# Optimization experiments

Measured on AMD Instinct MI355X. Metric: run time of the kernel, lower is better.

## Reference

```python
import jax, jax.numpy as jnp
import numpy as np

B, N, N_IN, MSG_HID, MSG_OUT, N_HID, N_OUT, K = 32, 128, 16, 64, 64, 64, 16, 4
E = N * (N - 1)  # 16256 directed edges, fully connected w/o self-loops


def setup_inputs() -> dict:
    key = jax.random.key(0)
    ks = jax.random.split(key, 8)
    # one-hot relation matrices (NRI convention)
    rows, cols = np.where(np.ones((N, N)) - np.eye(N))
    eye = np.eye(N, dtype=np.float32)
    rel_rec = jnp.asarray(eye[rows])   # [E, N]
    rel_send = jnp.asarray(eye[cols])  # [E, N]
    s = 0.1  # weight init scale
    return {
        "inputs": jax.random.normal(ks[0], (B, N_IN, N), jnp.float32),
        "rel_rec": rel_rec,
        "rel_send": rel_send,
        "rel_types": jax.nn.softmax(jax.random.normal(ks[1], (B, E, K), jnp.float32), axis=-1),
        "W1": jax.random.normal(ks[2], (K, 2 * N_IN, MSG_HID), jnp.float32) * s,
        "b1": jnp.zeros((K, MSG_HID), jnp.float32),
        "W2": jax.random.normal(ks[3], (K, MSG_HID, MSG_OUT), jnp.float32) * s,
        "b2": jnp.zeros((K, MSG_OUT), jnp.float32),
        "Wo1": jax.random.normal(ks[4], (MSG_OUT + N_IN, N_HID), jnp.float32) * s,
        "bo1": jnp.zeros((N_HID,), jnp.float32),
        "Wo2": jax.random.normal(ks[5], (N_HID, N_HID), jnp.float32) * s,
        "bo2": jnp.zeros((N_HID,), jnp.float32),
        "Wo3": jax.random.normal(ks[6], (N_HID, N_OUT), jnp.float32) * s,
        "bo3": jnp.zeros((N_OUT,), jnp.float32),
    }


def reference(inputs, rel_rec, rel_send, rel_types, W1, b1, W2, b2, Wo1, bo1, Wo2, bo2, Wo3, bo3):
    x = jnp.transpose(inputs, (0, 2, 1))                     # [B, N, n_in]
    senders = jnp.einsum('en,bnf->bef', rel_send, x)          # [B, E, n_in]
    receivers = jnp.einsum('en,bnf->bef', rel_rec, x)         # [B, E, n_in]
    pre_msg = jnp.concatenate([senders, receivers], axis=-1)  # [B, E, 2*n_in]
    all_msgs = jnp.zeros((pre_msg.shape[0], pre_msg.shape[1], W2.shape[-1]), pre_msg.dtype)
    for k in range(W1.shape[0]):  # small fixed loop over edge types
        m = jax.nn.relu(pre_msg @ W1[k] + b1[k])
        m = jax.nn.relu(m @ W2[k] + b2[k])
        all_msgs = all_msgs + m * rel_types[:, :, k:k + 1]
    # edge2node aggregation (no normalization in forward path, matches source)
    agg_msgs = jnp.einsum('bem,en->bnm', all_msgs, rel_rec)   # [B, N, msg_out]
    aug_msgs = jnp.concatenate([x, agg_msgs], axis=-1)        # [B, N, n_in+msg_out]
    h = jax.nn.relu(aug_msgs @ Wo1 + bo1)  # dropout disabled (eval mode)
    h = jax.nn.relu(h @ Wo2 + bo2)
    pred = h @ Wo3 + bo3                                      # [B, N, n_out]
    return jnp.transpose(pred, (0, 2, 1))                     # [B, n_out, N]
```

## Files before the change

### kernel.cpp

```cpp
#include <hip/hip_runtime.h>
#include <stdint.h>

#define B_  32
#define N_  128
#define NIN 16
#define K_  4
#define E_  (N_*(N_-1))

typedef float    f4 __attribute__((ext_vector_type(4)));
typedef _Float16 h8 __attribute__((ext_vector_type(8)));

__global__ __launch_bounds__(256) void prep(
    const float* __restrict__ inp, const float* __restrict__ W1,
    const float* __restrict__ b1,  const float* __restrict__ W2,
    const float* __restrict__ rt,
    _Float16* __restrict__ Sh, _Float16* __restrict__ Rh,
    _Float16* __restrict__ w2h, float* __restrict__ rtp)
{
    const int bid = blockIdx.x;
    const int tid = threadIdx.x;
    if (bid < 4096) {
        int gid = bid*256 + tid;
        int c = gid & 63;
        int n = (gid >> 6) & 127;
        int b = (gid >> 13) & 31;
        int k = gid >> 18;
        float s = 0.f, r = 0.f;
        const float* w1s = W1 + (k*32)*64 + c;
        const float* w1r = W1 + (k*32 + 16)*64 + c;
        const float* xp  = inp + (b*NIN)*N_ + n;
        #pragma unroll
        for (int f = 0; f < 16; ++f) {
            float xv = xp[f*N_];
            s += xv * w1s[f*64];
            r += xv * w1r[f*64];
        }
        r += b1[k*64 + c];
        Sh[gid] = (_Float16)s;
        Rh[gid] = (_Float16)r;
    } else if (bid < 4160) {
        int t = (bid - 4096)*256 + tid;
        int i    = t & 7;
        int lane = (t >> 3) & 63;
        int nt   = (t >> 9) & 3;
        int ks   = (t >> 11) & 1;
        int k    = t >> 12;
        int c = ks*32 + (lane >> 4)*8 + i;
        int o = nt*16 + (lane & 15);
        w2h[t] = (_Float16)W2[(k*64 + c)*64 + o];
    } else {
        int t = (bid - 4160)*256 + tid;
        int j = t & 127;
        int r = (t >> 7) & 127;
        int b = (t >> 14) & 31;
        int k = t >> 19;
        float v = 0.f;
        if (j < 127) v = rt[(b*E_ + r*127 + j)*4 + k];
        rtp[t] = v;
    }
}

__global__ __launch_bounds__(256) void edge_node(
    const _Float16* __restrict__ Sh, const _Float16* __restrict__ Rh,
    const _Float16* __restrict__ w2h, const float* __restrict__ rtp,
    const float* __restrict__ inp, const float* __restrict__ b2,
    const float* __restrict__ Wo1, const float* __restrict__ bo1,
    const float* __restrict__ Wo2, const float* __restrict__ bo2,
    const float* __restrict__ Wo3, const float* __restrict__ bo3,
    float* __restrict__ out)
{
    __shared__ float aggK[4*64];
    __shared__ float aug[80];
    __shared__ float psum[4][64];
    __shared__ float h1s[64];
    __shared__ float h2s[64];

    const int tid  = threadIdx.x;
    const int r    = blockIdx.x & 127;
    const int b    = blockIdx.x >> 7;
    const int k    = tid >> 6;
    const int lane = tid & 63;
    const int col  = lane & 15;
    const int q    = lane >> 4;

    if (tid < 16) aug[tid] = inp[(b*NIN + tid)*N_ + r];

    const h8* w2v = (const h8*)w2h;
    h8 w2f[2][4];
    #pragma unroll
    for (int ks = 0; ks < 2; ++ks)
        #pragma unroll
        for (int nt = 0; nt < 4; ++nt)
            w2f[ks][nt] = w2v[((k*2 + ks)*4 + nt)*64 + lane];

    const h8* Sv = (const h8*)Sh;
    const h8* Rv = (const h8*)Rh;
    const int rowR = ((k*B_ + b)*N_ + r) * 8;
    h8 rf0 = Rv[rowR + q];
    h8 rf1 = Rv[rowR + 4 + q];

    f4 b2i[4];
    #pragma unroll
    for (int nt = 0; nt < 4; ++nt) {
        float v = b2[k*64 + nt*16 + col];
        b2i[nt][0] = v; b2i[nt][1] = v; b2i[nt][2] = v; b2i[nt][3] = v;
    }

    float aggacc[4] = {0.f, 0.f, 0.f, 0.f};
    const int rowSbase = (k*B_ + b)*N_*8;
    const float* rtrow = rtp + ((k*B_ + b)*N_ + r)*128;
    const h8 zero8 = {0,0,0,0,0,0,0,0};

    #pragma unroll
    for (int mt = 0; mt < 8; ++mt) {
        int j = mt*16 + col;
        int s = j + (j >= r ? 1 : 0);
        if (s > 127) s = 127;
        h8 a0 = Sv[rowSbase + s*8 + q]     + rf0;
        h8 a1 = Sv[rowSbase + s*8 + 4 + q] + rf1;
        a0 = __builtin_elementwise_max(a0, zero8);
        a1 = __builtin_elementwise_max(a1, zero8);

        f4 rtv = *(const f4*)(rtrow + mt*16 + q*4);

        #pragma unroll
        for (int nt = 0; nt < 4; ++nt) {
            f4 acc = __builtin_amdgcn_mfma_f32_16x16x32_f16(a0, w2f[0][nt], b2i[nt], 0, 0, 0);
            acc     = __builtin_amdgcn_mfma_f32_16x16x32_f16(a1, w2f[1][nt], acc,    0, 0, 0);
            #pragma unroll
            for (int i = 0; i < 4; ++i)
                aggacc[nt] += rtv[i] * fmaxf(acc[i], 0.f);
        }
    }

    #pragma unroll
    for (int nt = 0; nt < 4; ++nt) {
        float v = aggacc[nt];
        v += __shfl_xor(v, 16, 64);
        v += __shfl_xor(v, 32, 64);
        if (lane < 16) aggK[k*64 + nt*16 + lane] = v;
    }
    __syncthreads();

    if (tid < 64)
        aug[16 + tid] = aggK[tid] + aggK[64 + tid] + aggK[128 + tid] + aggK[192 + tid];
    __syncthreads();

    {
        int o = tid & 63, p = tid >> 6;
        float s = 0.f;
        #pragma unroll
        for (int i = p*20; i < p*20 + 20; ++i) s += aug[i] * Wo1[i*64 + o];
        psum[p][o] = s;
    }
    __syncthreads();
    if (tid < 64)
        h1s[tid] = fmaxf(psum[0][tid] + psum[1][tid] + psum[2][tid] + psum[3][tid] + bo1[tid], 0.f);
    __syncthreads();

    {
        int o = tid & 63, p = tid >> 6;
        float s = 0.f;
        #pragma unroll
        for (int i = p*16; i < p*16 + 16; ++i) s += h1s[i] * Wo2[i*64 + o];
        psum[p][o] = s;
    }
    __syncthreads();
    if (tid < 64)
        h2s[tid] = fmaxf(psum[0][tid] + psum[1][tid] + psum[2][tid] + psum[3][tid] + bo2[tid], 0.f);
    __syncthreads();

    if (tid < 64) {
        int o = tid & 15, p = tid >> 4;
        float s = 0.f;
        #pragma unroll
        for (int i = p*16; i < p*16 + 16; ++i) s += h2s[i] * Wo3[i*16 + o];
        psum[p][o] = s;
    }
    __syncthreads();
    if (tid < 16)
        out[(b*NIN + tid)*N_ + r] =
            psum[0][tid] + psum[1][tid] + psum[2][tid] + psum[3][tid] + bo3[tid];
}

extern "C" void kernel_launch(void* const* d_in, const int* in_sizes, int n_in,
                              void* d_out, int out_size, void* d_ws, size_t ws_size,
                              hipStream_t stream)
{
    const float* inp = (const float*)d_in[0];
    const float* rt  = (const float*)d_in[3];
    const float* W1  = (const float*)d_in[4];
    const float* b1  = (const float*)d_in[5];
    const float* W2  = (const float*)d_in[6];
    const float* b2  = (const float*)d_in[7];
    const float* Wo1 = (const float*)d_in[8];
    const float* bo1 = (const float*)d_in[9];
    const float* Wo2 = (const float*)d_in[10];
    const float* bo2 = (const float*)d_in[11];
    const float* Wo3 = (const float*)d_in[12];
    const float* bo3 = (const float*)d_in[13];

    _Float16* Sh  = (_Float16*)d_ws;
    _Float16* Rh  = Sh + (1u << 20);
    _Float16* w2h = Rh + (1u << 20);
    float*    rtp = (float*)(w2h + 16384);

    hipLaunchKernelGGL(prep, dim3(12352), dim3(256), 0, stream,
                       inp, W1, b1, W2, rt, Sh, Rh, w2h, rtp);
    hipLaunchKernelGGL(edge_node, dim3(B_*N_), dim3(256), 0, stream,
                       Sh, Rh, w2h, rtp, inp, b2,
                       Wo1, bo1, Wo2, bo2, Wo3, bo3, (float*)d_out);
}
```

Baseline: 164.7 us.

## Split edge MFMA and node MLP kernels, reuse sender fragments across four receivers

The edge kernel now handles four receiver nodes per 512-thread block. It keeps sender fragments in registers and reuses them across receivers. The self-edge is zeroed in rel_types and indexed by sender, so the per-element index remap is gone. The relation-type weights are stored in fp16 to halve that traffic. The node MLP moves into a separate lightweight 64-thread kernel that reads aggregates from a workspace buffer, at the cost of an extra launch, an extra global round trip, and lower precision for the rel_types weights.

```diff
diff --git a/kernel.cpp b/kernel.cpp
--- a/kernel.cpp
+++ b/kernel.cpp
@@ -9,13 +9,14 @@
 
 typedef float    f4 __attribute__((ext_vector_type(4)));
 typedef _Float16 h8 __attribute__((ext_vector_type(8)));
+typedef _Float16 h4 __attribute__((ext_vector_type(4)));
 
 __global__ __launch_bounds__(256) void prep(
     const float* __restrict__ inp, const float* __restrict__ W1,
     const float* __restrict__ b1,  const float* __restrict__ W2,
     const float* __restrict__ rt,
     _Float16* __restrict__ Sh, _Float16* __restrict__ Rh,
-    _Float16* __restrict__ w2h, float* __restrict__ rtp)
+    _Float16* __restrict__ w2h, _Float16* __restrict__ rtn)
 {
     const int bid = blockIdx.x;
     const int tid = threadIdx.x;
@@ -50,137 +51,147 @@
         w2h[t] = (_Float16)W2[(k*64 + c)*64 + o];
     } else {
         int t = (bid - 4160)*256 + tid;
-        int j = t & 127;
+        int s = t & 127;
         int r = (t >> 7) & 127;
         int b = (t >> 14) & 31;
         int k = t >> 19;
-        float v = 0.f;
-        if (j < 127) v = rt[(b*E_ + r*127 + j)*4 + k];
-        rtp[t] = v;
-    }
-}
-
-__global__ __launch_bounds__(256) void edge_node(
+        _Float16 v = (_Float16)0.f;
+        if (s != r) {
+            int j = s - (s > r ? 1 : 0);
+            v = (_Float16)rt[(b*E_ + r*127 + j)*4 + k];
+        }
+        rtn[t] = v;
+    }
+}
+
+__global__ __launch_bounds__(512, 4) void edge_mfma(
     const _Float16* __restrict__ Sh, const _Float16* __restrict__ Rh,
-    const _Float16* __restrict__ w2h, const float* __restrict__ rtp,
-    const float* __restrict__ inp, const float* __restrict__ b2,
+    const _Float16* __restrict__ w2h, const _Float16* __restrict__ rtn,
+    const float* __restrict__ b2, float* __restrict__ agg)
+{
+    __shared__ float aggW[8][4][64];
+
+    const int tid  = threadIdx.x;
+    const int wave = tid >> 6;
+    const int k    = wave >> 1;
+    const int m0   = (wave & 1)*64;
+    const int lane = tid & 63;
+    const int col  = lane & 15;
+    const int q    = lane >> 4;
+    const int b     = blockIdx.x >> 5;
+    const int rbase = (blockIdx.x & 31)*4;
+    const int kb    = k*B_ + b;
+
+    const h8* Sv  = (const h8*)Sh;
+    const h8* Rv  = (const h8*)Rh;
+    const h8* w2v = (const h8*)w2h;
+
+    h8 sf[4][2];
+    #pragma unroll
+    for (int mt = 0; mt < 4; ++mt) {
+        int row = (kb*N_ + m0 + mt*16 + col)*8;
+        sf[mt][0] = Sv[row + q];
+        sf[mt][1] = Sv[row + 4 + q];
+    }
+
+    h8 w2f[2][4];
+    #pragma unroll
+    for (int ks = 0; ks < 2; ++ks)
+        #pragma unroll
+        for (int nt = 0; nt < 4; ++nt)
+            w2f[ks][nt] = w2v[((k*2 + ks)*4 + nt)*64 + lane];
+
+    f4 b2i[4];
+    #pragma unroll
+    for (int nt = 0; nt < 4; ++nt) {
+        float v = b2[k*64 + nt*16 + col];
+        b2i[nt][0] = v; b2i[nt][1] = v; b2i[nt][2] = v; b2i[nt][3] = v;
+    }
+
+    const h8 zero8 = {0,0,0,0,0,0,0,0};
+
+    #pragma unroll
+    for (int rg = 0; rg < 4; ++rg) {
+        const int r    = rbase + rg;
+        const int rowR = (kb*N_ + r)*8;
+        h8 rf0 = Rv[rowR + q];
+        h8 rf1 = Rv[rowR + 4 + q];
+        const h4* rtp = (const h4*)(rtn + (kb*N_ + r)*N_ + m0);
+
+        float aggacc[4] = {0.f, 0.f, 0.f, 0.f};
+        #pragma unroll
+        for (int mt = 0; mt < 4; ++mt) {
+            h8 a0 = __builtin_elementwise_max(sf[mt][0] + rf0, zero8);
+            h8 a1 = __builtin_elementwise_max(sf[mt][1] + rf1, zero8);
+            h4 rth = rtp[mt*4 + q];
+            float rtv[4];
+            #pragma unroll
+            for (int i = 0; i < 4; ++i) rtv[i] = (float)rth[i];
+
+            #pragma unroll
+            for (int nt = 0; nt < 4; ++nt) {
+                f4 acc = __builtin_amdgcn_mfma_f32_16x16x32_f16(a0, w2f[0][nt], b2i[nt], 0, 0, 0);
+                acc     = __builtin_amdgcn_mfma_f32_16x16x32_f16(a1, w2f[1][nt], acc,    0, 0, 0);
+                #pragma unroll
+                for (int i = 0; i < 4; ++i)
+                    aggacc[nt] += rtv[i] * fmaxf(acc[i], 0.f);
+            }
+        }
+        #pragma unroll
+        for (int nt = 0; nt < 4; ++nt) {
+            float v = aggacc[nt];
+            v += __shfl_xor(v, 16, 64);
+            v += __shfl_xor(v, 32, 64);
+            if (lane < 16) aggW[wave][rg][nt*16 + lane] = v;
+        }
+    }
+    __syncthreads();
+
+    if (tid < 256) {
+        int rg = tid >> 6, c = tid & 63;
+        float s = 0.f;
+        #pragma unroll
+        for (int w = 0; w < 8; ++w) s += aggW[w][rg][c];
+        agg[(b*N_ + rbase + rg)*64 + c] = s;
+    }
+}
+
+__global__ __launch_bounds__(64) void node_mlp(
+    const float* __restrict__ agg, const float* __restrict__ inp,
     const float* __restrict__ Wo1, const float* __restrict__ bo1,
     const float* __restrict__ Wo2, const float* __restrict__ bo2,
     const float* __restrict__ Wo3, const float* __restrict__ bo3,
     float* __restrict__ out)
 {
-    __shared__ float aggK[4*64];
     __shared__ float aug[80];
-    __shared__ float psum[4][64];
-    __shared__ float h1s[64];
-    __shared__ float h2s[64];
-
-    const int tid  = threadIdx.x;
-    const int r    = blockIdx.x & 127;
-    const int b    = blockIdx.x >> 7;
-    const int k    = tid >> 6;
-    const int lane = tid & 63;
-    const int col  = lane & 15;
-    const int q    = lane >> 4;
+    __shared__ float h1[64];
+    __shared__ float h2[64];
+    const int tid = threadIdx.x;
+    const int b = blockIdx.x >> 7;
+    const int r = blockIdx.x & 127;
 
     if (tid < 16) aug[tid] = inp[(b*NIN + tid)*N_ + r];
-
-    const h8* w2v = (const h8*)w2h;
-    h8 w2f[2][4];
-    #pragma unroll
-    for (int ks = 0; ks < 2; ++ks)
-        #pragma unroll
-        for (int nt = 0; nt < 4; ++nt)
-            w2f[ks][nt] = w2v[((k*2 + ks)*4 + nt)*64 + lane];
-
-    const h8* Sv = (const h8*)Sh;
-    const h8* Rv = (const h8*)Rh;
-    const int rowR = ((k*B_ + b)*N_ + r) * 8;
-    h8 rf0 = Rv[rowR + q];
-    h8 rf1 = Rv[rowR + 4 + q];
-
-    f4 b2i[4];
-    #pragma unroll
-    for (int nt = 0; nt < 4; ++nt) {
-        float v = b2[k*64 + nt*16 + col];
-        b2i[nt][0] = v; b2i[nt][1] = v; b2i[nt][2] = v; b2i[nt][3] = v;
-    }
-
-    float aggacc[4] = {0.f, 0.f, 0.f, 0.f};
-    const int rowSbase = (k*B_ + b)*N_*8;
-    const float* rtrow = rtp + ((k*B_ + b)*N_ + r)*128;
-    const h8 zero8 = {0,0,0,0,0,0,0,0};
-
-    #pragma unroll
-    for (int mt = 0; mt < 8; ++mt) {
-        int j = mt*16 + col;
-        int s = j + (j >= r ? 1 : 0);
-        if (s > 127) s = 127;
-        h8 a0 = Sv[rowSbase + s*8 + q]     + rf0;
-        h8 a1 = Sv[rowSbase + s*8 + 4 + q] + rf1;
-        a0 = __builtin_elementwise_max(a0, zero8);
-        a1 = __builtin_elementwise_max(a1, zero8);
-
-        f4 rtv = *(const f4*)(rtrow + mt*16 + q*4);
-
-        #pragma unroll
-        for (int nt = 0; nt < 4; ++nt) {
-            f4 acc = __builtin_amdgcn_mfma_f32_16x16x32_f16(a0, w2f[0][nt], b2i[nt], 0, 0, 0);
-            acc     = __builtin_amdgcn_mfma_f32_16x16x32_f16(a1, w2f[1][nt], acc,    0, 0, 0);
-            #pragma unroll
-            for (int i = 0; i < 4; ++i)
-                aggacc[nt] += rtv[i] * fmaxf(acc[i], 0.f);
-        }
-    }
-
-    #pragma unroll
-    for (int nt = 0; nt < 4; ++nt) {
-        float v = aggacc[nt];
-        v += __shfl_xor(v, 16, 64);
-        v += __shfl_xor(v, 32, 64);
-        if (lane < 16) aggK[k*64 + nt*16 + lane] = v;
-    }
-    __syncthreads();
-
-    if (tid < 64)
-        aug[16 + tid] = aggK[tid] + aggK[64 + tid] + aggK[128 + tid] + aggK[192 + tid];
-    __syncthreads();
-
-    {
-        int o = tid & 63, p = tid >> 6;
-        float s = 0.f;
-        #pragma unroll
-        for (int i = p*20; i < p*20 + 20; ++i) s += aug[i] * Wo1[i*64 + o];
-        psum[p][o] = s;
-    }
-    __syncthreads();
-    if (tid < 64)
-        h1s[tid] = fmaxf(psum[0][tid] + psum[1][tid] + psum[2][tid] + psum[3][tid] + bo1[tid], 0.f);
-    __syncthreads();
-
-    {
-        int o = tid & 63, p = tid >> 6;
-        float s = 0.f;
-        #pragma unroll
-        for (int i = p*16; i < p*16 + 16; ++i) s += h1s[i] * Wo2[i*64 + o];
-        psum[p][o] = s;
-    }
-    __syncthreads();
-    if (tid < 64)
-        h2s[tid] = fmaxf(psum[0][tid] + psum[1][tid] + psum[2][tid] + psum[3][tid] + bo2[tid], 0.f);
-    __syncthreads();
-
-    if (tid < 64) {
-        int o = tid & 15, p = tid >> 4;
-        float s = 0.f;
-        #pragma unroll
-        for (int i = p*16; i < p*16 + 16; ++i) s += h2s[i] * Wo3[i*16 + o];
-        psum[p][o] = s;
-    }
-    __syncthreads();
-    if (tid < 16)
-        out[(b*NIN + tid)*N_ + r] =
-            psum[0][tid] + psum[1][tid] + psum[2][tid] + psum[3][tid] + bo3[tid];
+    aug[16 + tid] = agg[(b*N_ + r)*64 + tid];
+    __syncthreads();
+
+    float s = bo1[tid];
+    #pragma unroll 8
+    for (int i = 0; i < 80; ++i) s += aug[i] * Wo1[i*64 + tid];
+    h1[tid] = fmaxf(s, 0.f);
+    __syncthreads();
+
+    s = bo2[tid];
+    #pragma unroll 8
+    for (int i = 0; i < 64; ++i) s += h1[i] * Wo2[i*64 + tid];
+    h2[tid] = fmaxf(s, 0.f);
+    __syncthreads();
+
+    if (tid < 16) {
+        s = bo3[tid];
+        #pragma unroll 8
+        for (int i = 0; i < 64; ++i) s += h2[i] * Wo3[i*16 + tid];
+        out[(b*NIN + tid)*N_ + r] = s;
+    }
 }
 
 extern "C" void kernel_launch(void* const* d_in, const int* in_sizes, int n_in,
@@ -203,11 +214,13 @@
     _Float16* Sh  = (_Float16*)d_ws;
     _Float16* Rh  = Sh + (1u << 20);
     _Float16* w2h = Rh + (1u << 20);
-    float*    rtp = (float*)(w2h + 16384);
+    _Float16* rtn = w2h + 16384;
+    float*    agg = (float*)(rtn + (1u << 21));
 
     hipLaunchKernelGGL(prep, dim3(12352), dim3(256), 0, stream,
-                       inp, W1, b1, W2, rt, Sh, Rh, w2h, rtp);
-    hipLaunchKernelGGL(edge_node, dim3(B_*N_), dim3(256), 0, stream,
-                       Sh, Rh, w2h, rtp, inp, b2,
-                       Wo1, bo1, Wo2, bo2, Wo3, bo3, (float*)d_out);
-}
+                       inp, W1, b1, W2, rt, Sh, Rh, w2h, rtn);
+    hipLaunchKernelGGL(edge_mfma, dim3(B_*N_/4), dim3(512), 0, stream,
+                       Sh, Rh, w2h, rtn, b2, agg);
+    hipLaunchKernelGGL(node_mlp, dim3(B_*N_), dim3(64), 0, stream,
+                       agg, inp, Wo1, bo1, Wo2, bo2, Wo3, bo3, (float*)d_out);
+}
```

Result: slower. 230.1 us (+39.7%).
